# Kernel tuning notes

Measured on AMD Instinct MI355X. Metric: run time of the kernel, lower is better.

Reference implementation:

```python
import jax, jax.numpy as jnp
import numpy as np

H, W = 64, 64
B, P, F = 8, 512, 512
EXPAND = 0.02      # bbox expansion for soft silhouette (NDC units), DIB-R default
MULT = 1000.0      # DIB-R coordinate multiplier
DELTA = 7000.0     # soft prob falloff in multiplier-scaled squared units, DIB-R default
EPS = 1e-10


def setup_inputs() -> dict:
    key = jax.random.key(0)
    k1, k2, k3 = jax.random.split(key, 3)
    verts = 0.5 * jax.random.normal(k1, (B, P, 3), dtype=jnp.float32)
    faces = jax.random.randint(k2, (B, F, 3), 0, P, dtype=jnp.int32)
    colors = jax.random.uniform(k3, (B, P, 3), dtype=jnp.float32)
    camera_rot = jnp.tile(jnp.eye(3, dtype=jnp.float32)[None], (B, 1, 1))
    camera_pos = jnp.tile(jnp.array([0.0, 0.0, 3.0], dtype=jnp.float32)[None], (B, 1))
    fov_factor = 2.7475  # 1 / tan(fovy/2), fovy ~ 0.7 rad, aspect 1
    camera_proj = jnp.array([[fov_factor], [fov_factor], [-1.0]], dtype=jnp.float32)
    return {"verts": verts, "faces": faces, "camera_rot": camera_rot,
            "camera_pos": camera_pos, "camera_proj": camera_proj, "colors": colors}


def _render_one(verts_p3, faces_f3, rot_33, pos_3, proj_31, colors_p3):
    # --- perspective_projection (pixel2mesh convention: p' = rot^T (p - pos)) ---
    pcam = (verts_p3 - pos_3[None, :]) @ rot_33.T                 # [P,3] camera frame
    xy3 = pcam * proj_31.reshape(3)[None, :]
    xy = xy3[:, :2] / xy3[:, 2:3]                                  # [P,2] NDC
    tri3d = pcam[faces_f3]                                         # [F,3,3]
    tri2d = xy[faces_f3]                                           # [F,3,2]
    normal = jnp.cross(tri3d[:, 1] - tri3d[:, 0], tri3d[:, 2] - tri3d[:, 0])  # [F,3]
    normalz = normal[:, 2]
    normal1 = normal / (jnp.linalg.norm(normal, axis=1, keepdims=True) + 1e-12)
    # per-face vertex colors + hard-mask channel -> [F,3,4] (== color_1xfx12)
    cmask = jnp.ones((faces_f3.shape[0], 3, 1), dtype=colors_p3.dtype)
    cfeat = jnp.concatenate([colors_p3[faces_f3], cmask], axis=2)

    # --- linear_rasterizer: pixel grid in NDC ---
    xs = (2.0 * jnp.arange(W, dtype=jnp.float32) + 1.0 - W) / W
    ys = (H - 2.0 * jnp.arange(H, dtype=jnp.float32) - 1.0) / H
    x0 = xs[None, :, None]                                         # [1,W,1]
    y0 = ys[:, None, None]                                         # [H,1,1]
    ax, ay = tri2d[:, 0, 0], tri2d[:, 0, 1]
    bx, by = tri2d[:, 1, 0], tri2d[:, 1, 1]
    cx, cy = tri2d[:, 2, 0], tri2d[:, 2, 1]
    det = (by - cy) * (ax - cx) + (cx - bx) * (ay - cy)            # [F]
    det_safe = jnp.where(jnp.abs(det) < EPS, EPS, det)
    w0 = ((by - cy) * (x0 - cx) + (cx - bx) * (y0 - cy)) / det_safe  # [H,W,F]
    w1 = ((cy - ay) * (x0 - cx) + (ax - cx) * (y0 - cy)) / det_safe
    w2 = 1.0 - w0 - w1
    z = w0 * tri3d[:, 0, 2] + w1 * tri3d[:, 1, 2] + w2 * tri3d[:, 2, 2]  # [H,W,F]
    covered = (w0 >= 0) & (w1 >= 0) & (w2 >= 0)
    valid = covered & (normalz > 0) & (jnp.abs(det) > EPS)
    # hard z-buffer: camera looks along -z, so nearest face has max z
    zbuf = jnp.where(valid, z, -1e10)
    best = jnp.argmax(zbuf, axis=-1)                               # [H,W]
    anyv = jnp.any(valid, axis=-1)
    gw = lambda w: jnp.take_along_axis(w, best[..., None], axis=-1)[..., 0]
    g0, g1, g2 = gw(w0), gw(w1), gw(w2)
    cb = cfeat[best]                                               # [H,W,3,4]
    feat = (g0[..., None] * cb[..., 0, :] + g1[..., None] * cb[..., 1, :]
            + g2[..., None] * cb[..., 2, :])
    imfeat = jnp.where(anyv[..., None], feat, 0.0)                 # [H,W,4]

    # --- soft silhouette probability ---
    def seg_d2(px, py, qx, qy):
        vx, vy = qx - px, qy - py
        t = jnp.clip(((x0 - px) * vx + (y0 - py) * vy)
                     / (vx * vx + vy * vy + 1e-12), 0.0, 1.0)
        dx, dy = x0 - (px + t * vx), y0 - (py + t * vy)
        return dx * dx + dy * dy
    d2 = jnp.minimum(jnp.minimum(seg_d2(ax, ay, bx, by), seg_d2(bx, by, cx, cy)),
                     seg_d2(cx, cy, ax, ay))
    d2 = jnp.where(covered, 0.0, d2)                               # inside -> 0
    xmin = jnp.minimum(jnp.minimum(ax, bx), cx) - EXPAND
    xmax = jnp.maximum(jnp.maximum(ax, bx), cx) + EXPAND
    ymin = jnp.minimum(jnp.minimum(ay, by), cy) - EXPAND
    ymax = jnp.maximum(jnp.maximum(ay, by), cy) + EXPAND
    in_bbox = (x0 >= xmin) & (x0 <= xmax) & (y0 >= ymin) & (y0 <= ymax)
    contrib = jnp.where(in_bbox, jnp.exp(-d2 * (MULT * MULT) / DELTA), 0.0)
    improb = 1.0 - jnp.prod(1.0 - contrib, axis=-1, keepdims=True)  # [H,W,1]
    return imfeat, improb, normal1


def reference(verts, faces, camera_rot, camera_pos, camera_proj, colors):
    imfeat, improb, normal1 = jax.vmap(_render_one, in_axes=(0, 0, 0, 0, None, 0))(
        verts, faces, camera_rot, camera_pos, camera_proj, colors)
    imrender = imfeat[..., :3]     # [B,H,W,3]
    hardmask = imfeat[..., 3:]     # [B,H,W,1]
    return imrender, improb, normal1, hardmask
```

## Files before the change

### kernel.cpp

```cpp
#include <hip/hip_runtime.h>
#include <math.h>

#define NB 8
#define NP 512
#define NF 512
#define NH 64
#define NW 64
#define FEXPAND 0.02f
#define FEPS 1e-10f

#define IMG_OFF 0
#define PROB_OFF (NB*NH*NW*3)
#define NRM_OFF  (PROB_OFF + NB*NH*NW)
#define MASK_OFF (NRM_OFF + NB*NF*3)

__global__ __launch_bounds__(1024, 8) void render_all(
    const float* __restrict__ verts, const int* __restrict__ faces,
    const float* __restrict__ rot, const float* __restrict__ pos,
    const float* __restrict__ proj, const float* __restrict__ colors,
    float* __restrict__ out)
{
  __shared__ __align__(16) float smem[NF*32];
  int tid  = threadIdx.x;
  int b    = blockIdx.x >> 6;
  int tile = blockIdx.x & 63;
  int wave = tid >> 6;
  int lane = tid & 63;
  int ix = (tile & 7)*8 + (lane & 7);
  int iy = (tile >> 3)*8 + (lane >> 3);
  float x = (2.0f*ix + 1.0f - 64.0f) * (1.0f/64.0f);
  float y = (64.0f - 2.0f*iy - 1.0f) * (1.0f/64.0f);

  if (tid < NF) {
    int t = b * NF + tid;
    float p0 = proj[0], p1 = proj[1], p2 = proj[2];
    float R0=rot[b*9+0],R1=rot[b*9+1],R2=rot[b*9+2];
    float R3=rot[b*9+3],R4=rot[b*9+4],R5=rot[b*9+5];
    float R6=rot[b*9+6],R7=rot[b*9+7],R8=rot[b*9+8];
    float ppx=pos[b*3+0], ppy=pos[b*3+1], ppz=pos[b*3+2];
    int idxs[3] = { faces[t*3+0], faces[t*3+1], faces[t*3+2] };
    float X[3],Y[3],Z[3],SX[3],SY[3];
#pragma unroll
    for (int k = 0; k < 3; ++k) {
      const float* v = verts + ((size_t)b*NP + idxs[k])*3;
      float dx = v[0]-ppx, dy = v[1]-ppy, dz = v[2]-ppz;
      float pcx = __fadd_rn(__fadd_rn(__fmul_rn(R0,dx),__fmul_rn(R1,dy)),__fmul_rn(R2,dz));
      float pcy = __fadd_rn(__fadd_rn(__fmul_rn(R3,dx),__fmul_rn(R4,dy)),__fmul_rn(R5,dz));
      float pcz = __fadd_rn(__fadd_rn(__fmul_rn(R6,dx),__fmul_rn(R7,dy)),__fmul_rn(R8,dz));
      X[k]=pcx; Y[k]=pcy; Z[k]=pcz;
      float dn = __fmul_rn(pcz, p2);
      SX[k] = __fdiv_rn(__fmul_rn(pcx, p0), dn);
      SY[k] = __fdiv_rn(__fmul_rn(pcy, p1), dn);
    }
    float e1x=X[1]-X[0], e1y=Y[1]-Y[0], e1z=Z[1]-Z[0];
    float e2x=X[2]-X[0], e2y=Y[2]-Y[0], e2z=Z[2]-Z[0];
    float nzel = __fsub_rn(__fmul_rn(e1x,e2y), __fmul_rn(e1y,e2x));
    if (tile == 0) {
      float m0 = __fmul_rn(e1z, e2y); float nxf = __fmaf_rn(e1y, e2z, -m0);
      float m1 = __fmul_rn(e1x, e2z); float nyf = __fmaf_rn(e1z, e2x, -m1);
      float m2 = __fmul_rn(e1y, e2x); float nzf = __fmaf_rn(e1x, e2y, -m2);
      float nn = __fsqrt_rn(__fadd_rn(__fadd_rn(__fmul_rn(nxf,nxf),__fmul_rn(nyf,nyf)),
                                      __fmul_rn(nzf,nzf)));
      float den = __fadd_rn(nn, 1e-12f);
      out[NRM_OFF + (size_t)t*3+0] = __fdiv_rn(nxf, den);
      out[NRM_OFF + (size_t)t*3+1] = __fdiv_rn(nyf, den);
      out[NRM_OFF + (size_t)t*3+2] = __fdiv_rn(nzf, den);
    }
    float ax=SX[0],ay=SY[0],bx=SX[1],by=SY[1],cx=SX[2],cy=SY[2];
    float det = __fadd_rn(__fmul_rn(__fsub_rn(by,cy),__fsub_rn(ax,cx)),
                          __fmul_rn(__fsub_rn(cx,bx),__fsub_rn(ay,cy)));
    float det_safe = (fabsf(det) < FEPS) ? FEPS : det;
    float validf = ((nzel > 0.0f) && (fabsf(det) > FEPS)) ? 1.0f : 0.0f;
    float* d = &smem[tid*32];
    d[0]=__fsub_rn(by,cy); d[1]=__fsub_rn(cx,bx);
    d[2]=__fsub_rn(cy,ay); d[3]=__fsub_rn(ax,cx);
    d[4]=cx; d[5]=cy; d[6]=det_safe; d[7]=validf;
    d[8]=Z[0]; d[9]=Z[1]; d[10]=Z[2];
    float vx=bx-ax, vy=by-ay;
    d[11]=1.0f/(vx*vx+vy*vy+1e-12f);
    d[20]=vx; d[21]=vy;
    d[12]=fminf(fminf(ax,bx),cx)-FEXPAND; d[13]=fmaxf(fmaxf(ax,bx),cx)+FEXPAND;
    d[14]=fminf(fminf(ay,by),cy)-FEXPAND; d[15]=fmaxf(fmaxf(ay,by),cy)+FEXPAND;
    d[16]=ax; d[17]=ay; d[18]=bx; d[19]=by;
    vx=cx-bx; vy=cy-by;
    d[22]=vx; d[23]=vy; d[26]=1.0f/(vx*vx+vy*vy+1e-12f);
    vx=ax-cx; vy=ay-cy;
    d[24]=vx; d[25]=vy; d[27]=1.0f/(vx*vx+vy*vy+1e-12f);
    d[28]=0.0f; d[29]=0.0f; d[30]=0.0f; d[31]=0.0f;
  }
  __syncthreads();

  float bestz = -1e10f;
  int   bestf = 0;
  float bw0 = 0.0f, bw1 = 0.0f, bw2 = 0.0f;
  float prod  = 1.0f;

  float4 bb = *(const float4*)&smem[wave*32 + 12];
  for (int j = 0; j < 32; ++j) {
    int f = (j << 4) + wave;
    float4 bbn = bb;
    if (j < 31) bbn = *(const float4*)&smem[(f + 16)*32 + 12];
    bool inb = (x >= bb.x) && (x <= bb.y) && (y >= bb.z) && (y <= bb.w);
    if (__any(inb)) {
      const float* r = &smem[f*32];
      float4 qe = *(const float4*)(r);
      float4 q1 = *(const float4*)(r + 4);
      float dxc = x - q1.x, dyc = y - q1.y;
      float n0 = __fadd_rn(__fmul_rn(qe.x, dxc), __fmul_rn(qe.y, dyc));
      float n1 = __fadd_rn(__fmul_rn(qe.z, dxc), __fmul_rn(qe.w, dyc));
      bool dsp  = q1.z > 0.0f;
      bool pass = ((n0 == 0.0f) || ((n0 > 0.0f) == dsp)) &&
                  ((n1 == 0.0f) || ((n1 > 0.0f) == dsp));
      bool act = inb && pass;
      bool covered = false;
      if (__any(act)) {
        float4 q2 = *(const float4*)(r + 8);
        float w0 = __fdiv_rn(n0, q1.z);
        float w1 = __fdiv_rn(n1, q1.z);
        float w2 = __fsub_rn(__fsub_rn(1.0f, w0), w1);
        covered = act && (w2 >= 0.0f);
        bool valid = covered && (q1.w > 0.5f);
        float z = __fadd_rn(__fadd_rn(__fmul_rn(w0,q2.x), __fmul_rn(w1,q2.y)),
                            __fmul_rn(w2,q2.z));
        float zval = valid ? z : -1e10f;
        if (zval > bestz) { bestz = zval; bestf = f; bw0 = w0; bw1 = w1; bw2 = w2; }
      }
      if (covered) prod = 0.0f;
      bool needd = inb && !covered && (prod != 0.0f);
      if (__any(needd)) {
        float4 qa = *(const float4*)(r + 16);
        float4 qv = *(const float4*)(r + 20);
        float4 qw = *(const float4*)(r + 24);
        float invAB = r[11];
        float dxa = x - qa.x, dya = y - qa.y;
        float t1 = fminf(fmaxf((dxa*qv.x + dya*qv.y)*invAB, 0.0f), 1.0f);
        float rx = dxa - t1*qv.x, ry = dya - t1*qv.y;
        float d2 = rx*rx + ry*ry;
        float dxb = x - qa.z, dyb = y - qa.w;
        t1 = fminf(fmaxf((dxb*qv.z + dyb*qv.w)*qw.z, 0.0f), 1.0f);
        rx = dxb - t1*qv.z; ry = dyb - t1*qv.w;
        d2 = fminf(d2, rx*rx + ry*ry);
        t1 = fminf(fmaxf((dxc*qw.x + dyc*qw.y)*qw.w, 0.0f), 1.0f);
        rx = dxc - t1*qw.x; ry = dyc - t1*qw.y;
        d2 = fminf(d2, rx*rx + ry*ry);
        if (needd)
          prod *= (1.0f - __expf(d2 * -142.85714285714286f));
      }
    }
    bb = bbn;
  }

  __syncthreads();
  float* comb = smem;
  float* c = comb + (size_t)(wave*64 + lane)*7;
  c[0]=bestz; c[1]=__int_as_float(bestf); c[2]=prod;
  c[3]=bw0; c[4]=bw1; c[5]=bw2;
  __syncthreads();

  if (tid < 64) {
    const float* c0 = comb + (size_t)tid*7;
    float bz = c0[0]; int bf = __float_as_int(c0[1]); float pr = c0[2];
    float w0 = c0[3], w1 = c0[4], w2 = c0[5];
    for (int s = 1; s < 16; ++s) {
      const float* cs = comb + (size_t)(s*64 + tid)*7;
      float oz = cs[0]; int of = __float_as_int(cs[1]);
      if (oz > bz || (oz == bz && of < bf)) { bz = oz; bf = of; w0 = cs[3]; w1 = cs[4]; w2 = cs[5]; }
      pr *= cs[2];
    }
    int av = (bz != -1e10f);
    int t = b * NF + bf;
    const int* fi = faces + (size_t)t*3;
    const float* cb = colors + (size_t)b*NP*3;
    int i0 = fi[0], i1 = fi[1], i2 = fi[2];
    float fr  = w0*cb[i0*3+0] + w1*cb[i1*3+0] + w2*cb[i2*3+0];
    float fgc = w0*cb[i0*3+1] + w1*cb[i1*3+1] + w2*cb[i2*3+1];
    float fb  = w0*cb[i0*3+2] + w1*cb[i1*3+2] + w2*cb[i2*3+2];
    float fa  = __fadd_rn(__fadd_rn(w0, w1), w2);
    int gp = b*4096 + iy*64 + ix;
    out[IMG_OFF + (size_t)gp*3 + 0] = av ? fr  : 0.0f;
    out[IMG_OFF + (size_t)gp*3 + 1] = av ? fgc : 0.0f;
    out[IMG_OFF + (size_t)gp*3 + 2] = av ? fb  : 0.0f;
    out[PROB_OFF + gp] = 1.0f - pr;
    out[MASK_OFF + gp] = av ? fa : 0.0f;
  }
}

extern "C" void kernel_launch(void* const* d_in, const int* in_sizes, int n_in,
                              void* d_out, int out_size, void* d_ws, size_t ws_size,
                              hipStream_t stream) {
  const float* verts  = (const float*)d_in[0];
  const int*   faces  = (const int*)  d_in[1];
  const float* rot    = (const float*)d_in[2];
  const float* pos    = (const float*)d_in[3];
  const float* proj   = (const float*)d_in[4];
  const float* colors = (const float*)d_in[5];
  float* out = (float*)d_out;
  (void)d_ws; (void)ws_size;

  hipLaunchKernelGGL(render_all, dim3(NB*64), dim3(1024), 0, stream,
                     verts, faces, rot, pos, proj, colors, out);
}
```

Before: 92.05 us.

## Cull faces per tile into a compacted list before rasterization loop

Each block tests every face's expanded bbox against its 8x8 pixel tile, compacts the overlapping face indices into a shared list via ballot/popcount prefix sums, and has the waves iterate only over that list instead of all 512 faces. The face record stride also shrinks from 32 to 28 floats. This is meant to cut loop iterations and bbox checks for faces that cannot touch the tile, at the cost of extra barriers and an indirect index load per iteration. The 28-float stride breaks 16-byte alignment for some float4 loads only when offsets are not multiples of 4, but 28 is a multiple of 4, so alignment holds.

```diff
diff --git a/kernel.cpp b/kernel.cpp
--- a/kernel.cpp
+++ b/kernel.cpp
@@ -20,16 +20,24 @@
     const float* __restrict__ proj, const float* __restrict__ colors,
     float* __restrict__ out)
 {
-  __shared__ __align__(16) float smem[NF*32];
+  __shared__ __align__(16) float smem[NF*28];
+  __shared__ unsigned short flist[NF];
+  __shared__ int wcnt[8];
+  __shared__ int Ltot;
   int tid  = threadIdx.x;
   int b    = blockIdx.x >> 6;
   int tile = blockIdx.x & 63;
   int wave = tid >> 6;
   int lane = tid & 63;
-  int ix = (tile & 7)*8 + (lane & 7);
-  int iy = (tile >> 3)*8 + (lane >> 3);
+  int ix0 = (tile & 7)*8, iy0 = (tile >> 3)*8;
+  int ix = ix0 + (lane & 7);
+  int iy = iy0 + (lane >> 3);
   float x = (2.0f*ix + 1.0f - 64.0f) * (1.0f/64.0f);
   float y = (64.0f - 2.0f*iy - 1.0f) * (1.0f/64.0f);
+  float txlo = (2.0f*ix0 + 1.0f - 64.0f) * (1.0f/64.0f);
+  float txhi = (2.0f*(ix0+7) + 1.0f - 64.0f) * (1.0f/64.0f);
+  float tyhi = (64.0f - 2.0f*iy0 - 1.0f) * (1.0f/64.0f);
+  float tylo = (64.0f - 2.0f*(iy0+7) - 1.0f) * (1.0f/64.0f);
 
   if (tid < NF) {
     int t = b * NF + tid;
@@ -71,7 +79,7 @@
                           __fmul_rn(__fsub_rn(cx,bx),__fsub_rn(ay,cy)));
     float det_safe = (fabsf(det) < FEPS) ? FEPS : det;
     float validf = ((nzel > 0.0f) && (fabsf(det) > FEPS)) ? 1.0f : 0.0f;
-    float* d = &smem[tid*32];
+    float* d = &smem[tid*28];
     d[0]=__fsub_rn(by,cy); d[1]=__fsub_rn(cx,bx);
     d[2]=__fsub_rn(cy,ay); d[3]=__fsub_rn(ax,cx);
     d[4]=cx; d[5]=cy; d[6]=det_safe; d[7]=validf;
@@ -86,33 +94,65 @@
     d[22]=vx; d[23]=vy; d[26]=1.0f/(vx*vx+vy*vy+1e-12f);
     vx=ax-cx; vy=ay-cy;
     d[24]=vx; d[25]=vy; d[27]=1.0f/(vx*vx+vy*vy+1e-12f);
-    d[28]=0.0f; d[29]=0.0f; d[30]=0.0f; d[31]=0.0f;
-  }
-  __syncthreads();
+  }
+  __syncthreads();
+
+  bool pass = false;
+  if (tid < NF) {
+    const float* rr = &smem[tid*28 + 12];
+    pass = (rr[1] >= txlo) && (rr[0] <= txhi) && (rr[3] >= tylo) && (rr[2] <= tyhi);
+  }
+  unsigned long long m = __ballot(pass);
+  if (tid < NF && (tid & 63) == 0) wcnt[tid >> 6] = __popcll(m);
+  __syncthreads();
+  if (tid < NF && pass) {
+    int w8 = tid >> 6;
+    int off = 0;
+#pragma unroll
+    for (int i = 0; i < 8; ++i) if (i < w8) off += wcnt[i];
+    off += __popcll(m & ((1ull << (tid & 63)) - 1ull));
+    flist[off] = (unsigned short)tid;
+  }
+  if (tid == 0) {
+    int s = 0;
+#pragma unroll
+    for (int i = 0; i < 8; ++i) s += wcnt[i];
+    Ltot = s;
+  }
+  __syncthreads();
+  int L = Ltot;
 
   float bestz = -1e10f;
   int   bestf = 0;
   float bw0 = 0.0f, bw1 = 0.0f, bw2 = 0.0f;
   float prod  = 1.0f;
 
-  float4 bb = *(const float4*)&smem[wave*32 + 12];
-  for (int j = 0; j < 32; ++j) {
-    int f = (j << 4) + wave;
+  int idx = wave;
+  int fcur = (idx < L) ? (int)flist[idx] : 0;
+  float4 bb = (idx < L) ? *(const float4*)&smem[fcur*28 + 12]
+                        : make_float4(0.f,0.f,0.f,0.f);
+  while (idx < L) {
+    int nidx = idx + 16;
+    int fnext = fcur;
     float4 bbn = bb;
-    if (j < 31) bbn = *(const float4*)&smem[(f + 16)*32 + 12];
+    if (nidx < L) {
+      fnext = (int)flist[nidx];
+      bbn = *(const float4*)&smem[fnext*28 + 12];
+    }
+    int f = fcur;
+    const float* r = &smem[f*28];
     bool inb = (x >= bb.x) && (x <= bb.y) && (y >= bb.z) && (y <= bb.w);
+    bool covered = false;
     if (__any(inb)) {
-      const float* r = &smem[f*32];
       float4 qe = *(const float4*)(r);
       float4 q1 = *(const float4*)(r + 4);
       float dxc = x - q1.x, dyc = y - q1.y;
       float n0 = __fadd_rn(__fmul_rn(qe.x, dxc), __fmul_rn(qe.y, dyc));
       float n1 = __fadd_rn(__fmul_rn(qe.z, dxc), __fmul_rn(qe.w, dyc));
       bool dsp  = q1.z > 0.0f;
-      bool pass = ((n0 == 0.0f) || ((n0 > 0.0f) == dsp)) &&
-                  ((n1 == 0.0f) || ((n1 > 0.0f) == dsp));
-      bool act = inb && pass;
-      bool covered = false;
+      bool spass = ((n0 == 0.0f) || ((n0 > 0.0f) == dsp)) &&
+                   ((n1 == 0.0f) || ((n1 > 0.0f) == dsp));
+      bool act = inb && spass;
       if (__any(act)) {
         float4 q2 = *(const float4*)(r + 8);
         float w0 = __fdiv_rn(n0, q1.z);
@@ -147,7 +187,7 @@
           prod *= (1.0f - __expf(d2 * -142.85714285714286f));
       }
     }
-    bb = bbn;
+    idx = nidx; fcur = fnext; bb = bbn;
   }
 
   __syncthreads();
```

Result: faster. 89.46 us (-2.8%).
